# Optimization experiments

Hardware: AMD Instinct MI355X
Metric: run time of the kernel (lower is better)

## Reference

```python
import jax, jax.numpy as jnp
import numpy as np

DIM = 128
HEADS = 8
RBF_K = 16
N_LIG = 20000
N_PROT = 80000
E = 262144
HEAD_DIM = DIM // HEADS
SCALE = HEAD_DIM ** -0.5


def setup_inputs() -> dict:
    key = jax.random.key(0)
    ks = jax.random.split(key, 16)
    inp = {
        "ligand_x": jax.random.normal(ks[0], (N_LIG, DIM), dtype=jnp.float32),
        "protein_x": jax.random.normal(ks[1], (N_PROT, DIM), dtype=jnp.float32),
        "cross_edges": jax.random.randint(ks[2], (E, 2), 0, N_LIG, dtype=jnp.int64)
        if jax.config.jax_enable_x64 else jax.random.randint(ks[2], (E, 2), 0, N_LIG, dtype=jnp.int32),
        "cross_attr": jax.random.uniform(ks[3], (E, RBF_K), dtype=jnp.float32),
        "Wq": jax.random.normal(ks[4], (DIM, DIM), dtype=jnp.float32) * (DIM ** -0.5),
        "bq": jax.random.normal(ks[5], (DIM,), dtype=jnp.float32) * 0.02,
        "Wk": jax.random.normal(ks[6], (DIM, DIM), dtype=jnp.float32) * (DIM ** -0.5),
        "bk": jax.random.normal(ks[7], (DIM,), dtype=jnp.float32) * 0.02,
        "Wv": jax.random.normal(ks[8], (DIM, DIM), dtype=jnp.float32) * (DIM ** -0.5),
        "bv": jax.random.normal(ks[9], (DIM,), dtype=jnp.float32) * 0.02,
        "Wo": jax.random.normal(ks[10], (DIM, DIM), dtype=jnp.float32) * (DIM ** -0.5),
        "bo": jax.random.normal(ks[11], (DIM,), dtype=jnp.float32) * 0.02,
        "Wr": jax.random.normal(ks[12], (RBF_K, HEADS), dtype=jnp.float32) * (RBF_K ** -0.5),
        "br": jax.random.normal(ks[13], (HEADS,), dtype=jnp.float32) * 0.02,
        "lig_start": 0,
        "prot_start": 0,
    }
    return inp


def _heads(t):
    return t.reshape(t.shape[0], HEADS, HEAD_DIM)


def _cross_attend(q_nodes, k_nodes, v_nodes, dst_idx, src_idx, rbf_bias, n_dst):
    # gather per-edge q/k/v: [E, H, D]
    qe = q_nodes[dst_idx]
    ke = k_nodes[src_idx]
    ve = v_nodes[src_idx]
    logits = jnp.einsum("ehd,ehd->eh", qe, ke) * SCALE + rbf_bias  # [E, H]
    # segment softmax over edges grouped by destination node
    m = jax.ops.segment_max(logits, dst_idx, num_segments=n_dst)  # [N, H]
    ex = jnp.exp(logits - m[dst_idx])
    s = jax.ops.segment_sum(ex, dst_idx, num_segments=n_dst)  # [N, H]
    w = ex / (s[dst_idx] + 1e-8)  # [E, H]
    agg = jax.ops.segment_sum(w[:, :, None] * ve, dst_idx, num_segments=n_dst)
    return agg.reshape(n_dst, HEADS * HEAD_DIM)


def reference(ligand_x, protein_x, cross_edges, cross_attr, Wq, bq, Wk, bk, Wv, bv,
              Wo, bo, Wr, br, lig_start, prot_start):
    n_lig, n_prot = ligand_x.shape[0], protein_x.shape[0]
    q_l = _heads(ligand_x @ Wq + bq)
    k_p = _heads(protein_x @ Wk + bk)
    v_p = _heads(protein_x @ Wv + bv)
    q_p = _heads(protein_x @ Wq + bq)
    k_l = _heads(ligand_x @ Wk + bk)
    v_l = _heads(ligand_x @ Wv + bv)

    lig_local = cross_edges[:, 0] - lig_start
    prot_local = cross_edges[:, 1] - prot_start
    rbf_bias = cross_attr @ Wr + br  # [E, heads]

    lig_agg = _cross_attend(q_l, k_p, v_p, lig_local, prot_local, rbf_bias, n_lig)
    prot_agg = _cross_attend(q_p, k_l, v_l, prot_local, lig_local, rbf_bias, n_prot)

    ligand_out = lig_agg @ Wo + bo   # dropout is identity at inference
    protein_out = prot_agg @ Wo + bo
    return (ligand_out, protein_out)
```

## Files before the change

kernel.cpp:

```cpp
#include <hip/hip_runtime.h>
#include <hip/hip_bf16.h>

typedef unsigned short u16;
typedef __attribute__((ext_vector_type(8))) short short8;
typedef __attribute__((ext_vector_type(4))) float f32x4;

__device__ __forceinline__ float bf2f(u16 u){
  union { unsigned int i; float f; } c; c.i = ((unsigned int)u) << 16; return c.f;
}
__device__ __forceinline__ u16 f2bf(float f){
  union { float f; unsigned int i; } c; c.f = f;
  unsigned int x = c.i;
  return (u16)((x + 0x7FFFu + ((x >> 16) & 1u)) >> 16);
}

__device__ __forceinline__ int edge_get(const int* __restrict__ e32, int i64, int e, int c){
  int idx = 2 * e + c;
  return i64 ? e32[2 * idx] : e32[idx];
}

__global__ __launch_bounds__(256) void init_kernel(
    const u16* __restrict__ lig16, const int* __restrict__ e32,
    int* __restrict__ flags, int* __restrict__ cnt, int ntot)
{
  int tid = threadIdx.x;
  if (blockIdx.x == 0){
    if (tid < 64){
      int c = 0, nz = 0;
      #pragma unroll
      for (int j = 0; j < 4; j++){
        u16 u = lig16[(tid * 4 + j) * 2];
        int ex = (u >> 7) & 0xFF;
        if (ex >= 96 && ex < 160) c++;
        if (e32[(tid * 4 + j) * 2 + 1] != 0) nz++;
      }
      #pragma unroll
      for (int off = 1; off < 64; off <<= 1){
        c  += __shfl_xor(c, off);
        nz += __shfl_xor(nz, off);
      }
      if (tid == 0){
        flags[0] = (c < 128) ? 1 : 0;
        flags[1] = (nz == 0) ? 1 : 0;
      }
    }
  } else {
    int i = (blockIdx.x - 1) * 256 + tid;
    if (i < ntot) cnt[i] = 0;
  }
}

__global__ __launch_bounds__(256) void prep_w(
    const void* __restrict__ Wq, const void* __restrict__ Wk,
    const void* __restrict__ Wv, const void* __restrict__ Wo,
    const void* __restrict__ bq, const void* __restrict__ bk,
    const void* __restrict__ bv, const void* __restrict__ bo,
    u16* __restrict__ Wt, float* __restrict__ biasP, const int* __restrict__ flags)
{
  int mat = blockIdx.x, tid = threadIdx.x;
  const void* W = (mat == 0) ? Wq : (mat == 1) ? Wk : (mat == 2) ? Wv : Wo;
  const void* b = (mat == 0) ? bq : (mat == 1) ? bk : (mat == 2) ? bv : bo;
  int F = flags[0];
  u16* dst = Wt + mat * 16384;
  #pragma unroll 4
  for (int j = 0; j < 64; j++){
    int idx = tid + j * 256;
    u16 w = F ? f2bf(((const float*)W)[idx]) : ((const u16*)W)[idx];
    dst[(idx & 127) * 128 + (idx >> 7)] = w;
  }
  if (tid < 128)
    biasP[mat * 128 + tid] = F ? ((const float*)b)[tid] : bf2f(((const u16*)b)[tid]);
}

__global__ __launch_bounds__(256) void fat_qkv_ep(
    const void* __restrict__ A0, int M0, const void* __restrict__ A1, int M1, int mb0,
    const u16* __restrict__ Wt, const float* __restrict__ biasP,
    u16* __restrict__ O0b, u16* __restrict__ O1b, u16* __restrict__ O2b,
    const void* __restrict__ attr, const void* __restrict__ Wr,
    const void* __restrict__ br, float* __restrict__ ebias,
    const int* __restrict__ edges, const int* __restrict__ ls_p,
    const int* __restrict__ ps_p, int* __restrict__ cnt,
    int nlig, int E_, const int* __restrict__ flags)
{
  __shared__ __align__(16) char smem[34816];
  int tid = threadIdx.x;
  int F = flags[0];

  int TT = mb0 + ((M1 + 63) >> 6);
  int eb = (E_ + 255) >> 8;
  int G  = TT + eb;
  int bx = blockIdx.x;
  long long pp = (long long)bx * TT;
  int tile = (int)(pp / G);
  int isQ  = (int)(((long long)(bx + 1) * TT) / G) > tile;

  if (isQ){
    u16 (*As)[136] = (u16(*)[136])smem;
    u16 (*Fs)[136] = (u16(*)[136])(smem + 17408);
    int AF = F;
    const void* A; int M, m0, orow;
    if (tile < mb0){ A = A0; M = M0; m0 = tile * 64;          orow = m0; }
    else           { A = A1; M = M1; m0 = (tile - mb0) * 64;  orow = M0 + m0; }

    if (AF){
      const float* Af = (const float*)A;
      #pragma unroll
      for (int j = 0; j < 8; j++){
        int u = tid + j * 256, row = u >> 5, c4 = (u & 31) * 4;
        float4 v = make_float4(0.f, 0.f, 0.f, 0.f);
        if (m0 + row < M) v = *(const float4*)&Af[(size_t)(m0 + row) * 128 + c4];
        ushort4 o; o.x = f2bf(v.x); o.y = f2bf(v.y); o.z = f2bf(v.z); o.w = f2bf(v.w);
        *(ushort4*)&As[row][c4] = o;
      }
    } else {
      const float4* Au = (const float4*)A;
      #pragma unroll
      for (int j = 0; j < 4; j++){
        int u = tid + j * 256, row = u >> 4, c8 = (u & 15);
        float4 v = make_float4(0.f, 0.f, 0.f, 0.f);
        if (m0 + row < M) v = Au[(size_t)(m0 + row) * 16 + c8];
        *(float4*)&As[row][c8 * 8] = v;
      }
    }
    __syncthreads();

    int wave = tid >> 6, lane = tid & 63;
    int quad = lane >> 4, ml = lane & 15;

    for (int mat = 0; mat < 3; mat++){
      const u16* wp = Wt + (size_t)mat * 16384
                        + (size_t)(wave * 32 + ml) * 128 + quad * 8;
      short8 wf0[4], wf1[4];
      #pragma unroll
      for (int kk = 0; kk < 4; kk++){
        wf0[kk] = *(const short8*)&wp[kk * 32];
        wf1[kk] = *(const short8*)&wp[2048 + kk * 32];
      }
      float b0 = biasP[mat * 128 + wave * 32 + ml];
      float b1 = biasP[mat * 128 + wave * 32 + 16 + ml];

      f32x4 acc[4][2];
      #pragma unroll
      for (int mt = 0; mt < 4; mt++){
        acc[mt][0] = (f32x4){0.f, 0.f, 0.f, 0.f};
        acc[mt][1] = (f32x4){0.f, 0.f, 0.f, 0.f};
      }
      #pragma unroll
      for (int mt = 0; mt < 4; mt++){
        #pragma unroll
        for (int kk = 0; kk < 4; kk++){
          short8 af = *(const short8*)&As[mt * 16 + ml][kk * 32 + quad * 8];
          acc[mt][0] = __builtin_amdgcn_mfma_f32_16x16x32_bf16(af, wf0[kk], acc[mt][0], 0, 0, 0);
          acc[mt][1] = __builtin_amdgcn_mfma_f32_16x16x32_bf16(af, wf1[kk], acc[mt][1], 0, 0, 0);
        }
      }

      if (mat > 0) __syncthreads();
      #pragma unroll
      for (int mt = 0; mt < 4; mt++){
        #pragma unroll
        for (int r = 0; r < 4; r++){
          int row = mt * 16 + quad * 4 + r;
          Fs[row][wave * 32 + ml]      = f2bf(acc[mt][0][r] + b0);
          Fs[row][wave * 32 + 16 + ml] = f2bf(acc[mt][1][r] + b1);
        }
      }
      __syncthreads();
      u16* Cb = (mat == 0) ? O0b : ((mat == 1) ? O1b : O2b);
      #pragma unroll
      for (int j = 0; j < 4; j++){
        int u = tid + j * 256, row = u >> 4, c8 = (u & 15) * 8;
        if (m0 + row < M)
          *(short8*)&Cb[(size_t)(orow + row) * 128 + c8] = *(const short8*)&Fs[row][c8];
      }
    }
  } else {
    int eidx = bx - tile;
    float (*w)[8] = (float(*)[8])smem;
    float* b = (float*)(smem + 512);
    if (tid < 128) w[tid >> 3][tid & 7] = F ? ((const float*)Wr)[tid] : bf2f(((const u16*)Wr)[tid]);
    if (tid < 8)   b[tid] = F ? ((const float*)br)[tid] : bf2f(((const u16*)br)[tid]);
    __syncthreads();
    int e = eidx * 256 + tid;
    if (e >= E_) return;

    int I64 = flags[1];
    int dl = edge_get(edges, I64, e, 0) - ls_p[0];
    int dp = edge_get(edges, I64, e, 1) - ps_p[0];
    atomicAdd(&cnt[dl], 1);
    atomicAdd(&cnt[nlig + dp], 1);

    float a[16];
    if (F){
      const float* af = (const float*)attr;
      #pragma unroll
      for (int j = 0; j < 4; j++){
        float4 t = *(const float4*)&af[e * 16 + j * 4];
        a[4*j] = t.x; a[4*j+1] = t.y; a[4*j+2] = t.z; a[4*j+3] = t.w;
      }
    } else {
      const u16* au = (const u16*)attr;
      #pragma unroll
      for (int j = 0; j < 4; j++){
        ushort4 t = *(const ushort4*)&au[e * 16 + j * 4];
        a[4*j] = bf2f(t.x); a[4*j+1] = bf2f(t.y); a[4*j+2] = bf2f(t.z); a[4*j+3] = bf2f(t.w);
      }
    }
    #pragma unroll
    for (int hh = 0; hh < 8; hh++){
      float s = b[hh];
      #pragma unroll
      for (int r = 0; r < 16; r++) s += a[r] * w[r][hh];
      ebias[e * 8 + hh] = s;
    }
  }
}

__global__ __launch_bounds__(256) void gemm_multi(
    const void* __restrict__ A0, int M0, const void* __restrict__ A1, int M1, int mb0,
    const u16* __restrict__ Wt, const float* __restrict__ biasP, int wbase, int nm,
    u16* __restrict__ O0b, u16* __restrict__ O1b, u16* __restrict__ O2b,
    float* __restrict__ O0f,
    int a_force_bf16, int final_out, const int* __restrict__ flags)
{
  __shared__ __align__(16) u16 As[64][136];
  __shared__ __align__(16) u16 Fs[64][136];

  int tid = threadIdx.x;
  int F = flags[0];
  int AF = a_force_bf16 ? 0 : F;
  int xb = blockIdx.x;
  const void* A; int M, m0, orow;
  if (xb < mb0){ A = A0; M = M0; m0 = xb * 64;          orow = m0; }
  else         { A = A1; M = M1; m0 = (xb - mb0) * 64;  orow = M0 + m0; }

  if (AF){
    const float* Af = (const float*)A;
    #pragma unroll
    for (int j = 0; j < 8; j++){
      int u = tid + j * 256, row = u >> 5, c4 = (u & 31) * 4;
      float4 v = make_float4(0.f, 0.f, 0.f, 0.f);
      if (m0 + row < M) v = *(const float4*)&Af[(size_t)(m0 + row) * 128 + c4];
      ushort4 o; o.x = f2bf(v.x); o.y = f2bf(v.y); o.z = f2bf(v.z); o.w = f2bf(v.w);
      *(ushort4*)&As[row][c4] = o;
    }
  } else {
    const float4* Au = (const float4*)A;
    #pragma unroll
    for (int j = 0; j < 4; j++){
      int u = tid + j * 256, row = u >> 4, c8 = (u & 15);
      float4 v = make_float4(0.f, 0.f, 0.f, 0.f);
      if (m0 + row < M) v = Au[(size_t)(m0 + row) * 16 + c8];
      *(float4*)&As[row][c8 * 8] = v;
    }
  }
  __syncthreads();

  int wave = tid >> 6, lane = tid & 63;
  int quad = lane >> 4, ml = lane & 15;
  int f32out = final_out && F;

  for (int mat = 0; mat < nm; mat++){
    const u16* wp = Wt + (size_t)(wbase + mat) * 16384
                      + (size_t)(wave * 32 + ml) * 128 + quad * 8;
    short8 wf0[4], wf1[4];
    #pragma unroll
    for (int kk = 0; kk < 4; kk++){
      wf0[kk] = *(const short8*)&wp[kk * 32];
      wf1[kk] = *(const short8*)&wp[2048 + kk * 32];
    }
    float b0 = biasP[(wbase + mat) * 128 + wave * 32 + ml];
    float b1 = biasP[(wbase + mat) * 128 + wave * 32 + 16 + ml];

    f32x4 acc[4][2];
    #pragma unroll
    for (int mt = 0; mt < 4; mt++){
      acc[mt][0] = (f32x4){0.f, 0.f, 0.f, 0.f};
      acc[mt][1] = (f32x4){0.f, 0.f, 0.f, 0.f};
    }

    #pragma unroll
    for (int mt = 0; mt < 4; mt++){
      #pragma unroll
      for (int kk = 0; kk < 4; kk++){
        short8 af = *(const short8*)&As[mt * 16 + ml][kk * 32 + quad * 8];
        acc[mt][0] = __builtin_amdgcn_mfma_f32_16x16x32_bf16(af, wf0[kk], acc[mt][0], 0, 0, 0);
        acc[mt][1] = __builtin_amdgcn_mfma_f32_16x16x32_bf16(af, wf1[kk], acc[mt][1], 0, 0, 0);
      }
    }

    if (f32out){
      #pragma unroll
      for (int mt = 0; mt < 4; mt++){
        #pragma unroll
        for (int r = 0; r < 4; r++){
          int row = mt * 16 + quad * 4 + r;
          if (m0 + row < M){
            float* op = &O0f[(size_t)(orow + row) * 128 + wave * 32 + ml];
            op[0]  = acc[mt][0][r] + b0;
            op[16] = acc[mt][1][r] + b1;
          }
        }
      }
    } else {
      if (mat > 0) __syncthreads();
      #pragma unroll
      for (int mt = 0; mt < 4; mt++){
        #pragma unroll
        for (int r = 0; r < 4; r++){
          int row = mt * 16 + quad * 4 + r;
          Fs[row][wave * 32 + ml]      = f2bf(acc[mt][0][r] + b0);
          Fs[row][wave * 32 + 16 + ml] = f2bf(acc[mt][1][r] + b1);
        }
      }
      __syncthreads();
      u16* Cb = (mat == 0) ? O0b : ((mat == 1) ? O1b : O2b);
      #pragma unroll
      for (int j = 0; j < 4; j++){
        int u = tid + j * 256, row = u >> 4, c8 = (u & 15) * 8;
        if (m0 + row < M)
          *(short8*)&Cb[(size_t)(orow + row) * 128 + c8] = *(const short8*)&Fs[row][c8];
      }
    }
  }
}

__global__ __launch_bounds__(256) void scan_blocksum(
    const int* __restrict__ cnt, int* __restrict__ bsum, int n)
{
  __shared__ int red[4];
  int tid = threadIdx.x;
  int i = blockIdx.x * 256 + tid;
  int v = (i < n) ? cnt[i] : 0;
  #pragma unroll
  for (int off = 1; off < 64; off <<= 1) v += __shfl_xor(v, off);
  if ((tid & 63) == 0) red[tid >> 6] = v;
  __syncthreads();
  if (tid == 0) bsum[blockIdx.x] = red[0] + red[1] + red[2] + red[3];
}

__global__ __launch_bounds__(512) void scan_bsum(
    int* __restrict__ bsum, int* __restrict__ boff, int nb)
{
  __shared__ int buf[512];
  int tid = threadIdx.x;
  int v = (tid < nb) ? bsum[tid] : 0;
  buf[tid] = v; __syncthreads();
  for (int off = 1; off < 512; off <<= 1){
    int t = (tid >= off) ? buf[tid - off] : 0;
    __syncthreads();
    buf[tid] += t;
    __syncthreads();
  }
  if (tid < nb) boff[tid] = buf[tid] - v;
}

__global__ __launch_bounds__(256) void scan_final(
    const int* __restrict__ cnt, const int* __restrict__ boff,
    int* __restrict__ offs, int* __restrict__ cursor, int n)
{
  __shared__ int buf[256];
  int tid = threadIdx.x;
  int i = blockIdx.x * 256 + tid;
  int v = (i < n) ? cnt[i] : 0;
  buf[tid] = v; __syncthreads();
  for (int off = 1; off < 256; off <<= 1){
    int t = (tid >= off) ? buf[tid - off] : 0;
    __syncthreads();
    buf[tid] += t;
    __syncthreads();
  }
  int excl = buf[tid] - v + boff[blockIdx.x];
  if (i < n){
    offs[i] = excl;
    cursor[i] = excl;
    if (i == n - 1) offs[n] = excl + v;
  }
}

__global__ __launch_bounds__(256) void scatter_kernel(
    const int* __restrict__ edges, const int* __restrict__ ls_p,
    const int* __restrict__ ps_p, int* __restrict__ cursor,
    int2* __restrict__ sorted, int nlig, int E_,
    const int* __restrict__ flags)
{
  int e = blockIdx.x * 256 + threadIdx.x;
  if (e >= E_) return;
  int I64 = flags[1];
  int dl = edge_get(edges, I64, e, 0) - ls_p[0];
  int dp = edge_get(edges, I64, e, 1) - ps_p[0];
  int p1 = atomicAdd(&cursor[dl], 1);        sorted[p1] = make_int2(e, nlig + dp);
  int p2 = atomicAdd(&cursor[nlig + dp], 1); sorted[p2] = make_int2(e, dl);
}

__global__ __launch_bounds__(256) void attn_kernel(
    const u16* __restrict__ Q, const u16* __restrict__ K, const u16* __restrict__ V,
    const int2* __restrict__ sorted, const int* __restrict__ offs,
    const float* __restrict__ ebias, u16* __restrict__ AGG, int ntot)
{
  int t = blockIdx.x * 4 + (threadIdx.x >> 6);
  if (t >= ntot) return;
  int lane = threadIdx.x & 63;
  int ql = lane & 15;
  int q4 = lane >> 4;
  int h  = ql >> 1;

  int beg = offs[t], end = offs[t + 1];

  if (beg == end){
    if (lane < 16){
      short8 z = {0, 0, 0, 0, 0, 0, 0, 0};
      *(short8*)&AGG[(size_t)t * 128 + ql * 8] = z;
    }
    return;
  }

  short8 qv = *(const short8*)&Q[(size_t)t * 128 + ql * 8];
  float qf[8];
  #pragma unroll
  for (int j = 0; j < 8; j++) qf[j] = bf2f((u16)qv[j]);

  float m = -1e30f, l = 0.f;
  float a[8];
  #pragma unroll
  for (int j = 0; j < 8; j++) a[j] = 0.f;

  int i = beg + q4;
  int2 cur = make_int2(0, 0), nxt = make_int2(0, 0);
  if (i < end)     cur = sorted[i];
  if (i + 4 < end) nxt = sorted[i + 4];

  short8 kA = {0,0,0,0,0,0,0,0}, vA = {0,0,0,0,0,0,0,0};
  float ebA = 0.f;
  if (i < end){
    kA = *(const short8*)&K[(size_t)cur.y * 128 + ql * 8];
    vA = *(const short8*)&V[(size_t)cur.y * 128 + ql * 8];
    ebA = ebias[(size_t)cur.x * 8 + h];
  }

  while (i < end){
    short8 kB = {0,0,0,0,0,0,0,0}, vB = {0,0,0,0,0,0,0,0};
    float ebB = 0.f;
    if (i + 4 < end){
      kB = *(const short8*)&K[(size_t)nxt.y * 128 + ql * 8];
      vB = *(const short8*)&V[(size_t)nxt.y * 128 + ql * 8];
      ebB = ebias[(size_t)nxt.x * 8 + h];
    }
    int2 n2 = make_int2(0, 0);
    if (i + 8 < end) n2 = sorted[i + 8];

    float s = 0.f;
    #pragma unroll
    for (int j = 0; j < 8; j++) s += qf[j] * bf2f((u16)kA[j]);
    s += __shfl_xor(s, 1);
    float logit = s * 0.25f + ebA;
    float nm = fmaxf(m, logit);
    float alpha = __expf(m - nm);
    float p = __expf(logit - nm);
    #pragma unroll
    for (int j = 0; j < 8; j++) a[j] = a[j] * alpha + p * bf2f((u16)vA[j]);
    l = l * alpha + p;
    m = nm;

    kA = kB; vA = vB; ebA = ebB;
    cur = nxt; nxt = n2;
    i += 4;
  }

  #pragma unroll
  for (int mask = 16; mask <= 32; mask <<= 1){
    float mo = __shfl_xor(m, mask);
    float lo = __shfl_xor(l, mask);
    float nm = fmaxf(m, mo);
    float sA = __expf(m - nm);
    float sB = __expf(mo - nm);
    l = l * sA + lo * sB;
    #pragma unroll
    for (int j = 0; j < 8; j++){
      float ao = __shfl_xor(a[j], mask);
      a[j] = a[j] * sA + ao * sB;
    }
    m = nm;
  }

  if (lane < 16){
    float inv = 1.f / (l + 1e-8f);
    short8 o;
    #pragma unroll
    for (int j = 0; j < 8; j++) o[j] = (short)f2bf(a[j] * inv);
    *(short8*)&AGG[(size_t)t * 128 + ql * 8] = o;
  }
}

extern "C" void kernel_launch(void* const* d_in, const int* in_sizes, int n_in,
                              void* d_out, int out_size, void* d_ws, size_t ws_size,
                              hipStream_t stream)
{
  const void* ligand_x  = d_in[0];
  const void* protein_x = d_in[1];
  const int* edges      = (const int*)d_in[2];
  const void* attr      = d_in[3];
  const void* Wq = d_in[4];  const void* bq = d_in[5];
  const void* Wk = d_in[6];  const void* bk = d_in[7];
  const void* Wv = d_in[8];  const void* bv = d_in[9];
  const void* Wo = d_in[10]; const void* bo = d_in[11];
  const void* Wr = d_in[12]; const void* br = d_in[13];
  const int* ls_p = (const int*)d_in[14];
  const int* ps_p = (const int*)d_in[15];

  const int nlig = in_sizes[0] / 128;
  const int nprot = in_sizes[1] / 128;
  const int E = in_sizes[2] / 2;
  const int ntot = nlig + nprot;

  char* w = (char*)d_ws;
  size_t off = 0;
  auto alloc = [&](size_t bytes) -> void* {
    void* p = w + off;
    off = (off + bytes + 255) & ~(size_t)255;
    return p;
  };
  int*   flags = (int*)alloc(256);
  u16*   Wt    = (u16*)alloc(4 * 16384 * 2);
  float* biasP = (float*)alloc(4 * 128 * 4);
  u16* Qb  = (u16*)alloc((size_t)ntot * 128 * 2);
  u16* Kb  = (u16*)alloc((size_t)ntot * 128 * 2);
  u16* Vb  = (u16*)alloc((size_t)ntot * 128 * 2);
  u16* AGG = (u16*)alloc((size_t)ntot * 128 * 2);
  float* ebias = (float*)alloc((size_t)E * 8 * 4);
  int* cnt    = (int*)alloc((size_t)ntot * 4);
  int* offs   = (int*)alloc((size_t)(ntot + 1) * 4);
  int* cursor = (int*)alloc((size_t)ntot * 4);
  int* bsum   = (int*)alloc(512 * 4);
  int* boff   = (int*)alloc(512 * 4);
  int2* sorted = (int2*)alloc((size_t)2 * E * 8);
  (void)ws_size; (void)n_in; (void)out_size;

  const int mb_l = (nlig + 63) / 64;
  const int mb_p = (nprot + 63) / 64;
  const int mb_t = (ntot + 63) / 64;
  const int eb = (E + 255) / 256;
  const int nb = (ntot + 255) / 256;

  init_kernel<<<nb + 1, 256, 0, stream>>>((const u16*)ligand_x, edges, flags, cnt, ntot);

  prep_w<<<4, 256, 0, stream>>>(Wq, Wk, Wv, Wo, bq, bk, bv, bo, Wt, biasP, flags);

  const int TT = mb_l + mb_p;
  fat_qkv_ep<<<TT + eb, 256, 0, stream>>>(
      ligand_x, nlig, protein_x, nprot, mb_l,
      Wt, biasP, Qb, Kb, Vb,
      attr, Wr, br, ebias, edges, ls_p, ps_p, cnt, nlig, E, flags);

  scan_blocksum<<<nb, 256, 0, stream>>>(cnt, bsum, ntot);
  scan_bsum<<<1, 512, 0, stream>>>(bsum, boff, nb);
  scan_final<<<nb, 256, 0, stream>>>(cnt, boff, offs, cursor, ntot);
  scatter_kernel<<<eb, 256, 0, stream>>>(edges, ls_p, ps_p, cursor, sorted, nlig, E, flags);

  attn_kernel<<<(ntot + 3) / 4, 256, 0, stream>>>(Qb, Kb, Vb, sorted, offs, ebias, AGG, ntot);

  gemm_multi<<<mb_t, 256, 0, stream>>>(
      AGG, ntot, nullptr, 0, mb_t,
      Wt, biasP, 3, 1,
      (u16*)d_out, nullptr, nullptr, (float*)d_out,
      1, 1, flags);
}
```

Measured before the change: 319.5 us.

## Merge init kernels, split QKV projection per matrix, chained single-pass scan

Fuses the weight-prep kernel into the init kernel, with each weight block recomputing the dtype flag locally. The QKV projection grid now gives each block one (tile, matrix) pair instead of looping over three matrices, which triples the block count but reloads the A tile three times. The three-kernel prefix scan becomes one chained-scan kernel that passes block partials through spin-waiting atomics. The aim is fewer launches and better parallelism, at the cost of serialized look-back and extra input reads.

Result: slower. 379.4 us (+18.7%).

```diff
diff --git a/kernel.cpp b/kernel.cpp
--- a/kernel.cpp
+++ b/kernel.cpp
@@ -19,12 +19,47 @@
   return i64 ? e32[2 * idx] : e32[idx];
 }
 
-__global__ __launch_bounds__(256) void init_kernel(
+__global__ __launch_bounds__(256) void init_all(
+    const void* __restrict__ Wq, const void* __restrict__ Wk,
+    const void* __restrict__ Wv, const void* __restrict__ Wo,
+    const void* __restrict__ bq, const void* __restrict__ bk,
+    const void* __restrict__ bv, const void* __restrict__ bo,
+    u16* __restrict__ Wt, float* __restrict__ biasP,
     const u16* __restrict__ lig16, const int* __restrict__ e32,
-    int* __restrict__ flags, int* __restrict__ cnt, int ntot)
-{
-  int tid = threadIdx.x;
-  if (blockIdx.x == 0){
+    int* __restrict__ flags, int* __restrict__ partials,
+    int* __restrict__ cnt, int ntot)
+{
+  int bx = blockIdx.x, tid = threadIdx.x;
+
+  if (bx < 4){
+    __shared__ int Fsh;
+    if (tid < 64){
+      int c = 0;
+      #pragma unroll
+      for (int j = 0; j < 4; j++){
+        u16 u = lig16[(tid * 4 + j) * 2];
+        int ex = (u >> 7) & 0xFF;
+        if (ex >= 96 && ex < 160) c++;
+      }
+      #pragma unroll
+      for (int off = 1; off < 64; off <<= 1) c += __shfl_xor(c, off);
+      if (tid == 0) Fsh = (c < 128) ? 1 : 0;
+    }
+    __syncthreads();
+    int F = Fsh;
+    int mat = bx;
+    const void* W = (mat == 0) ? Wq : (mat == 1) ? Wk : (mat == 2) ? Wv : Wo;
+    const void* b = (mat == 0) ? bq : (mat == 1) ? bk : (mat == 2) ? bv : bo;
+    u16* dst = Wt + mat * 16384;
+    #pragma unroll 4
+    for (int j = 0; j < 64; j++){
+      int idx = tid + j * 256;
+      u16 w = F ? f2bf(((const float*)W)[idx]) : ((const u16*)W)[idx];
+      dst[(idx & 127) * 128 + (idx >> 7)] = w;
+    }
+    if (tid < 128)
+      biasP[mat * 128 + tid] = F ? ((const float*)b)[tid] : bf2f(((const u16*)b)[tid]);
+  } else if (bx == 4){
     if (tid < 64){
       int c = 0, nz = 0;
       #pragma unroll
@@ -44,32 +79,12 @@
         flags[1] = (nz == 0) ? 1 : 0;
       }
     }
+    partials[tid] = -1;
+    partials[256 + tid] = -1;
   } else {
-    int i = (blockIdx.x - 1) * 256 + tid;
+    int i = (bx - 5) * 256 + tid;
     if (i < ntot) cnt[i] = 0;
   }
-}
-
-__global__ __launch_bounds__(256) void prep_w(
-    const void* __restrict__ Wq, const void* __restrict__ Wk,
-    const void* __restrict__ Wv, const void* __restrict__ Wo,
-    const void* __restrict__ bq, const void* __restrict__ bk,
-    const void* __restrict__ bv, const void* __restrict__ bo,
-    u16* __restrict__ Wt, float* __restrict__ biasP, const int* __restrict__ flags)
-{
-  int mat = blockIdx.x, tid = threadIdx.x;
-  const void* W = (mat == 0) ? Wq : (mat == 1) ? Wk : (mat == 2) ? Wv : Wo;
-  const void* b = (mat == 0) ? bq : (mat == 1) ? bk : (mat == 2) ? bv : bo;
-  int F = flags[0];
-  u16* dst = Wt + mat * 16384;
-  #pragma unroll 4
-  for (int j = 0; j < 64; j++){
-    int idx = tid + j * 256;
-    u16 w = F ? f2bf(((const float*)W)[idx]) : ((const u16*)W)[idx];
-    dst[(idx & 127) * 128 + (idx >> 7)] = w;
-  }
-  if (tid < 128)
-    biasP[mat * 128 + tid] = F ? ((const float*)b)[tid] : bf2f(((const u16*)b)[tid]);
 }
 
 __global__ __launch_bounds__(256) void fat_qkv_ep(
@@ -88,13 +103,16 @@
 
   int TT = mb0 + ((M1 + 63) >> 6);
   int eb = (E_ + 255) >> 8;
-  int G  = TT + eb;
+  long long NQ = 3LL * TT;
+  int G  = (int)NQ + eb;
   int bx = blockIdx.x;
-  long long pp = (long long)bx * TT;
-  int tile = (int)(pp / G);
-  int isQ  = (int)(((long long)(bx + 1) * TT) / G) > tile;
+  long long q = ((long long)bx * NQ) / G;
+  int isQ = (int)(((long long)(bx + 1) * NQ) / G) > (int)q;
 
   if (isQ){
+    int qidx = (int)q;
+    int tile = qidx / 3;
+    int mat  = qidx - tile * 3;
     u16 (*As)[136] = (u16(*)[136])smem;
     u16 (*Fs)[136] = (u16(*)[136])(smem + 17408);
     int AF = F;
@@ -127,55 +145,52 @@
     int wave = tid >> 6, lane = tid & 63;
     int quad = lane >> 4, ml = lane & 15;
 
-    for (int mat = 0; mat < 3; mat++){
-      const u16* wp = Wt + (size_t)mat * 16384
-                        + (size_t)(wave * 32 + ml) * 128 + quad * 8;
-      short8 wf0[4], wf1[4];
+    const u16* wp = Wt + (size_t)mat * 16384
+                      + (size_t)(wave * 32 + ml) * 128 + quad * 8;
+    short8 wf0[4], wf1[4];
+    #pragma unroll
+    for (int kk = 0; kk < 4; kk++){
+      wf0[kk] = *(const short8*)&wp[kk * 32];
+      wf1[kk] = *(const short8*)&wp[2048 + kk * 32];
+    }
+    float b0 = biasP[mat * 128 + wave * 32 + ml];
+    float b1 = biasP[mat * 128 + wave * 32 + 16 + ml];
+
+    f32x4 acc[4][2];
+    #pragma unroll
+    for (int mt = 0; mt < 4; mt++){
+      acc[mt][0] = (f32x4){0.f, 0.f, 0.f, 0.f};
+      acc[mt][1] = (f32x4){0.f, 0.f, 0.f, 0.f};
+    }
+    #pragma unroll
+    for (int mt = 0; mt < 4; mt++){
       #pragma unroll
       for (int kk = 0; kk < 4; kk++){
-        wf0[kk] = *(const short8*)&wp[kk * 32];
-        wf1[kk] = *(const short8*)&wp[2048 + kk * 32];
-      }
-      float b0 = biasP[mat * 128 + wave * 32 + ml];
-      float b1 = biasP[mat * 128 + wave * 32 + 16 + ml];
-
-      f32x4 acc[4][2];
-      #pragma unroll
-      for (int mt = 0; mt < 4; mt++){
-        acc[mt][0] = (f32x4){0.f, 0.f, 0.f, 0.f};
-        acc[mt][1] = (f32x4){0.f, 0.f, 0.f, 0.f};
-      }
-      #pragma unroll
-      for (int mt = 0; mt < 4; mt++){
-        #pragma unroll
-        for (int kk = 0; kk < 4; kk++){
-          short8 af = *(const short8*)&As[mt * 16 + ml][kk * 32 + quad * 8];
-          acc[mt][0] = __builtin_amdgcn_mfma_f32_16x16x32_bf16(af, wf0[kk], acc[mt][0], 0, 0, 0);
-          acc[mt][1] = __builtin_amdgcn_mfma_f32_16x16x32_bf16(af, wf1[kk], acc[mt][1], 0, 0, 0);
-        }
-      }
-
-      if (mat > 0) __syncthreads();
-      #pragma unroll
-      for (int mt = 0; mt < 4; mt++){
-        #pragma unroll
-        for (int r = 0; r < 4; r++){
-          int row = mt * 16 + quad * 4 + r;
-          Fs[row][wave * 32 + ml]      = f2bf(acc[mt][0][r] + b0);
-          Fs[row][wave * 32 + 16 + ml] = f2bf(acc[mt][1][r] + b1);
-        }
-      }
-      __syncthreads();
-      u16* Cb = (mat == 0) ? O0b : ((mat == 1) ? O1b : O2b);
-      #pragma unroll
-      for (int j = 0; j < 4; j++){
-        int u = tid + j * 256, row = u >> 4, c8 = (u & 15) * 8;
-        if (m0 + row < M)
-          *(short8*)&Cb[(size_t)(orow + row) * 128 + c8] = *(const short8*)&Fs[row][c8];
-      }
+        short8 af = *(const short8*)&As[mt * 16 + ml][kk * 32 + quad * 8];
+        acc[mt][0] = __builtin_amdgcn_mfma_f32_16x16x32_bf16(af, wf0[kk], acc[mt][0], 0, 0, 0);
+        acc[mt][1] = __builtin_amdgcn_mfma_f32_16x16x32_bf16(af, wf1[kk], acc[mt][1], 0, 0, 0);
+      }
+    }
+
+    #pragma unroll
+    for (int mt = 0; mt < 4; mt++){
+      #pragma unroll
+      for (int r = 0; r < 4; r++){
+        int row = mt * 16 + quad * 4 + r;
+        Fs[row][wave * 32 + ml]      = f2bf(acc[mt][0][r] + b0);
+        Fs[row][wave * 32 + 16 + ml] = f2bf(acc[mt][1][r] + b1);
+      }
+    }
+    __syncthreads();
+    u16* Cb = (mat == 0) ? O0b : ((mat == 1) ? O1b : O2b);
+    #pragma unroll
+    for (int j = 0; j < 4; j++){
+      int u = tid + j * 256, row = u >> 4, c8 = (u & 15) * 8;
+      if (m0 + row < M)
+        *(short8*)&Cb[(size_t)(orow + row) * 128 + c8] = *(const short8*)&Fs[row][c8];
     }
   } else {
-    int eidx = bx - tile;
+    int eidx = bx - (int)q;
     float (*w)[8] = (float(*)[8])smem;
     float* b = (float*)(smem + 512);
     if (tid < 128) w[tid >> 3][tid & 7] = F ? ((const float*)Wr)[tid] : bf2f(((const u16*)Wr)[tid]);
@@ -213,6 +228,171 @@
       for (int r = 0; r < 16; r++) s += a[r] * w[r][hh];
       ebias[e * 8 + hh] = s;
     }
+  }
+}
+
+__global__ __launch_bounds__(256) void scan_chain(
+    const int* __restrict__ cnt, int* __restrict__ offs, int* __restrict__ cursor,
+    int* __restrict__ partials, int n)
+{
+  __shared__ int lds[256];
+  __shared__ int base_s;
+  int b = blockIdx.x, tid = threadIdx.x;
+  int i0 = b * 2048 + tid * 8;
+
+  int v[8]; int s = 0;
+  #pragma unroll
+  for (int j = 0; j < 8; j++){
+    int idx = i0 + j;
+    v[j] = (idx < n) ? cnt[idx] : 0;
+    s += v[j];
+  }
+  lds[tid] = s; __syncthreads();
+  for (int off = 1; off < 256; off <<= 1){
+    int t = (tid >= off) ? lds[tid - off] : 0;
+    __syncthreads();
+    lds[tid] += t;
+    __syncthreads();
+  }
+  int thr_excl = lds[tid] - s;
+  int block_sum = lds[255];
+
+  if (tid == 0){
+    int prev = 0;
+    if (b > 0){
+      while ((prev = __hip_atomic_load(&partials[b - 1], __ATOMIC_ACQUIRE,
+                                       __HIP_MEMORY_SCOPE_AGENT)) < 0){}
+    }
+    __hip_atomic_store(&partials[b], prev + block_sum, __ATOMIC_RELEASE,
+                       __HIP_MEMORY_SCOPE_AGENT);
+    base_s = prev;
+  }
+  __syncthreads();
+
+  int base = base_s + thr_excl;
+  #pragma unroll
+  for (int j = 0; j < 8; j++){
+    int idx = i0 + j;
+    if (idx < n){
+      offs[idx] = base;
+      cursor[idx] = base;
+      base += v[j];
+      if (idx == n - 1) offs[n] = base;
+    }
+  }
+}
+
+__global__ __launch_bounds__(256) void scatter_kernel(
+    const int* __restrict__ edges, const int* __restrict__ ls_p,
+    const int* __restrict__ ps_p, int* __restrict__ cursor,
+    int2* __restrict__ sorted, int nlig, int E_,
+    const int* __restrict__ flags)
+{
+  int e = blockIdx.x * 256 + threadIdx.x;
+  if (e >= E_) return;
+  int I64 = flags[1];
+  int dl = edge_get(edges, I64, e, 0) - ls_p[0];
+  int dp = edge_get(edges, I64, e, 1) - ps_p[0];
+  int p1 = atomicAdd(&cursor[dl], 1);        sorted[p1] = make_int2(e, nlig + dp);
+  int p2 = atomicAdd(&cursor[nlig + dp], 1); sorted[p2] = make_int2(e, dl);
+}
+
+__global__ __launch_bounds__(256) void attn_kernel(
+    const u16* __restrict__ Q, const u16* __restrict__ K, const u16* __restrict__ V,
+    const int2* __restrict__ sorted, const int* __restrict__ offs,
+    const float* __restrict__ ebias, u16* __restrict__ AGG, int ntot)
+{
+  int t = blockIdx.x * 4 + (threadIdx.x >> 6);
+  if (t >= ntot) return;
+  int lane = threadIdx.x & 63;
+  int ql = lane & 15;
+  int q4 = lane >> 4;
+  int h  = ql >> 1;
+
+  int beg = offs[t], end = offs[t + 1];
+
+  if (beg == end){
+    if (lane < 16){
+      short8 z = {0, 0, 0, 0, 0, 0, 0, 0};
+      *(short8*)&AGG[(size_t)t * 128 + ql * 8] = z;
+    }
+    return;
+  }
+
+  short8 qv = *(const short8*)&Q[(size_t)t * 128 + ql * 8];
+  float qf[8];
+  #pragma unroll
+  for (int j = 0; j < 8; j++) qf[j] = bf2f((u16)qv[j]);
+
+  float m = -1e30f, l = 0.f;
+  float a[8];
+  #pragma unroll
+  for (int j = 0; j < 8; j++) a[j] = 0.f;
+
+  int i = beg + q4;
+  int2 cur = make_int2(0, 0), nxt = make_int2(0, 0);
+  if (i < end)     cur = sorted[i];
+  if (i + 4 < end) nxt = sorted[i + 4];
+
+  short8 kA = {0,0,0,0,0,0,0,0}, vA = {0,0,0,0,0,0,0,0};
+  float ebA = 0.f;
+  if (i < end){
+    kA = *(const short8*)&K[(size_t)cur.y * 128 + ql * 8];
+    vA = *(const short8*)&V[(size_t)cur.y * 128 + ql * 8];
+    ebA = ebias[(size_t)cur.x * 8 + h];
+  }
+
+  while (i < end){
+    short8 kB = {0,0,0,0,0,0,0,0}, vB = {0,0,0,0,0,0,0,0};
+    float ebB = 0.f;
+    if (i + 4 < end){
+      kB = *(const short8*)&K[(size_t)nxt.y * 128 + ql * 8];
+      vB = *(const short8*)&V[(size_t)nxt.y * 128 + ql * 8];
+      ebB = ebias[(size_t)nxt.x * 8 + h];
+    }
+    int2 n2 = make_int2(0, 0);
+    if (i + 8 < end) n2 = sorted[i + 8];
+
+    float s = 0.f;
+    #pragma unroll
+    for (int j = 0; j < 8; j++) s += qf[j] * bf2f((u16)kA[j]);
+    s += __shfl_xor(s, 1);
+    float logit = s * 0.25f + ebA;
+    float nm = fmaxf(m, logit);
+    float alpha = __expf(m - nm);
+    float p = __expf(logit - nm);
+    #pragma unroll
+    for (int j = 0; j < 8; j++) a[j] = a[j] * alpha + p * bf2f((u16)vA[j]);
+    l = l * alpha + p;
+    m = nm;
+
+    kA = kB; vA = vB; ebA = ebB;
+    cur = nxt; nxt = n2;
+    i += 4;
+  }
+
+  #pragma unroll
+  for (int mask = 16; mask <= 32; mask <<= 1){
+    float mo = __shfl_xor(m, mask);
+    float lo = __shfl_xor(l, mask);
+    float nm = fmaxf(m, mo);
+    float sA = __expf(m - nm);
+    float sB = __expf(mo - nm);
+    l = l * sA + lo * sB;
+    #pragma unroll
+    for (int j = 0; j < 8; j++){
+      float ao = __shfl_xor(a[j], mask);
+      a[j] = a[j] * sA + ao * sB;
+    }
+    m = nm;
+  }
+
+  if (lane < 16){
+    float inv = 1.f / (l + 1e-8f);
+    short8 o;
+    #pragma unroll
+    for (int j = 0; j < 8; j++) o[j] = (short)f2bf(a[j] * inv);
+    *(short8*)&AGG[(size_t)t * 128 + ql * 8] = o;
   }
 }
 
@@ -322,173 +502,6 @@
           *(short8*)&Cb[(size_t)(orow + row) * 128 + c8] = *(const short8*)&Fs[row][c8];
       }
     }
-  }
-}
-
-__global__ __launch_bounds__(256) void scan_blocksum(
-    const int* __restrict__ cnt, int* __restrict__ bsum, int n)
-{
-  __shared__ int red[4];
-  int tid = threadIdx.x;
-  int i = blockIdx.x * 256 + tid;
-  int v = (i < n) ? cnt[i] : 0;
-  #pragma unroll
-  for (int off = 1; off < 64; off <<= 1) v += __shfl_xor(v, off);
-  if ((tid & 63) == 0) red[tid >> 6] = v;
-  __syncthreads();
-  if (tid == 0) bsum[blockIdx.x] = red[0] + red[1] + red[2] + red[3];
-}
-
-__global__ __launch_bounds__(512) void scan_bsum(
-    int* __restrict__ bsum, int* __restrict__ boff, int nb)
-{
-  __shared__ int buf[512];
-  int tid = threadIdx.x;
-  int v = (tid < nb) ? bsum[tid] : 0;
-  buf[tid] = v; __syncthreads();
-  for (int off = 1; off < 512; off <<= 1){
-    int t = (tid >= off) ? buf[tid - off] : 0;
-    __syncthreads();
-    buf[tid] += t;
-    __syncthreads();
-  }
-  if (tid < nb) boff[tid] = buf[tid] - v;
-}
-
-__global__ __launch_bounds__(256) void scan_final(
-    const int* __restrict__ cnt, const int* __restrict__ boff,
-    int* __restrict__ offs, int* __restrict__ cursor, int n)
-{
-  __shared__ int buf[256];
-  int tid = threadIdx.x;
-  int i = blockIdx.x * 256 + tid;
-  int v = (i < n) ? cnt[i] : 0;
-  buf[tid] = v; __syncthreads();
-  for (int off = 1; off < 256; off <<= 1){
-    int t = (tid >= off) ? buf[tid - off] : 0;
-    __syncthreads();
-    buf[tid] += t;
-    __syncthreads();
-  }
-  int excl = buf[tid] - v + boff[blockIdx.x];
-  if (i < n){
-    offs[i] = excl;
-    cursor[i] = excl;
-    if (i == n - 1) offs[n] = excl + v;
-  }
-}
-
-__global__ __launch_bounds__(256) void scatter_kernel(
-    const int* __restrict__ edges, const int* __restrict__ ls_p,
-    const int* __restrict__ ps_p, int* __restrict__ cursor,
-    int2* __restrict__ sorted, int nlig, int E_,
-    const int* __restrict__ flags)
-{
-  int e = blockIdx.x * 256 + threadIdx.x;
-  if (e >= E_) return;
-  int I64 = flags[1];
-  int dl = edge_get(edges, I64, e, 0) - ls_p[0];
-  int dp = edge_get(edges, I64, e, 1) - ps_p[0];
-  int p1 = atomicAdd(&cursor[dl], 1);        sorted[p1] = make_int2(e, nlig + dp);
-  int p2 = atomicAdd(&cursor[nlig + dp], 1); sorted[p2] = make_int2(e, dl);
-}
-
-__global__ __launch_bounds__(256) void attn_kernel(
-    const u16* __restrict__ Q, const u16* __restrict__ K, const u16* __restrict__ V,
-    const int2* __restrict__ sorted, const int* __restrict__ offs,
-    const float* __restrict__ ebias, u16* __restrict__ AGG, int ntot)
-{
-  int t = blockIdx.x * 4 + (threadIdx.x >> 6);
-  if (t >= ntot) return;
-  int lane = threadIdx.x & 63;
-  int ql = lane & 15;
-  int q4 = lane >> 4;
-  int h  = ql >> 1;
-
-  int beg = offs[t], end = offs[t + 1];
-
-  if (beg == end){
-    if (lane < 16){
-      short8 z = {0, 0, 0, 0, 0, 0, 0, 0};
-      *(short8*)&AGG[(size_t)t * 128 + ql * 8] = z;
-    }
-    return;
-  }
-
-  short8 qv = *(const short8*)&Q[(size_t)t * 128 + ql * 8];
-  float qf[8];
-  #pragma unroll
-  for (int j = 0; j < 8; j++) qf[j] = bf2f((u16)qv[j]);
-
-  float m = -1e30f, l = 0.f;
-  float a[8];
-  #pragma unroll
-  for (int j = 0; j < 8; j++) a[j] = 0.f;
-
-  int i = beg + q4;
-  int2 cur = make_int2(0, 0), nxt = make_int2(0, 0);
-  if (i < end)     cur = sorted[i];
-  if (i + 4 < end) nxt = sorted[i + 4];
-
-  short8 kA = {0,0,0,0,0,0,0,0}, vA = {0,0,0,0,0,0,0,0};
-  float ebA = 0.f;
-  if (i < end){
-    kA = *(const short8*)&K[(size_t)cur.y * 128 + ql * 8];
-    vA = *(const short8*)&V[(size_t)cur.y * 128 + ql * 8];
-    ebA = ebias[(size_t)cur.x * 8 + h];
-  }
-
-  while (i < end){
-    short8 kB = {0,0,0,0,0,0,0,0}, vB = {0,0,0,0,0,0,0,0};
-    float ebB = 0.f;
-    if (i + 4 < end){
-      kB = *(const short8*)&K[(size_t)nxt.y * 128 + ql * 8];
-      vB = *(const short8*)&V[(size_t)nxt.y * 128 + ql * 8];
-      ebB = ebias[(size_t)nxt.x * 8 + h];
-    }
-    int2 n2 = make_int2(0, 0);
-    if (i + 8 < end) n2 = sorted[i + 8];
-
-    float s = 0.f;
-    #pragma unroll
-    for (int j = 0; j < 8; j++) s += qf[j] * bf2f((u16)kA[j]);
-    s += __shfl_xor(s, 1);
-    float logit = s * 0.25f + ebA;
-    float nm = fmaxf(m, logit);
-    float alpha = __expf(m - nm);
-    float p = __expf(logit - nm);
-    #pragma unroll
-    for (int j = 0; j < 8; j++) a[j] = a[j] * alpha + p * bf2f((u16)vA[j]);
-    l = l * alpha + p;
-    m = nm;
-
-    kA = kB; vA = vB; ebA = ebB;
-    cur = nxt; nxt = n2;
-    i += 4;
-  }
-
-  #pragma unroll
-  for (int mask = 16; mask <= 32; mask <<= 1){
-    float mo = __shfl_xor(m, mask);
-    float lo = __shfl_xor(l, mask);
-    float nm = fmaxf(m, mo);
-    float sA = __expf(m - nm);
-    float sB = __expf(mo - nm);
-    l = l * sA + lo * sB;
-    #pragma unroll
-    for (int j = 0; j < 8; j++){
-      float ao = __shfl_xor(a[j], mask);
-      a[j] = a[j] * sA + ao * sB;
-    }
-    m = nm;
-  }
-
-  if (lane < 16){
-    float inv = 1.f / (l + 1e-8f);
-    short8 o;
-    #pragma unroll
-    for (int j = 0; j < 8; j++) o[j] = (short)f2bf(a[j] * inv);
-    *(short8*)&AGG[(size_t)t * 128 + ql * 8] = o;
   }
 }
 
@@ -528,11 +541,10 @@
   u16* Vb  = (u16*)alloc((size_t)ntot * 128 * 2);
   u16* AGG = (u16*)alloc((size_t)ntot * 128 * 2);
   float* ebias = (float*)alloc((size_t)E * 8 * 4);
-  int* cnt    = (int*)alloc((size_t)ntot * 4);
-  int* offs   = (int*)alloc((size_t)(ntot + 1) * 4);
-  int* cursor = (int*)alloc((size_t)ntot * 4);
-  int* bsum   = (int*)alloc(512 * 4);
-  int* boff   = (int*)alloc(512 * 4);
+  int* cnt      = (int*)alloc((size_t)ntot * 4);
+  int* offs     = (int*)alloc((size_t)(ntot + 1) * 4);
+  int* cursor   = (int*)alloc((size_t)ntot * 4);
+  int* partials = (int*)alloc(512 * 4);
   int2* sorted = (int2*)alloc((size_t)2 * E * 8);
   (void)ws_size; (void)n_in; (void)out_size;
 
@@ -541,20 +553,20 @@
   const int mb_t = (ntot + 63) / 64;
   const int eb = (E + 255) / 256;
   const int nb = (ntot + 255) / 256;
-
-  init_kernel<<<nb + 1, 256, 0, stream>>>((const u16*)ligand_x, edges, flags, cnt, ntot);
-
-  prep_w<<<4, 256, 0, stream>>>(Wq, Wk, Wv, Wo, bq, bk, bv, bo, Wt, biasP, flags);
+  const int nsb = (ntot + 2047) / 2048;
+
+  init_all<<<nb + 5, 256, 0, stream>>>(
+      Wq, Wk, Wv, Wo, bq, bk, bv, bo, Wt, biasP,
+      (const u16*)ligand_x, edges, flags, partials, cnt, ntot);
 
   const int TT = mb_l + mb_p;
-  fat_qkv_ep<<<TT + eb, 256, 0, stream>>>(
+  fat_qkv_ep<<<3 * TT + eb, 256, 0, stream>>>(
       ligand_x, nlig, protein_x, nprot, mb_l,
       Wt, biasP, Qb, Kb, Vb,
       attr, Wr, br, ebias, edges, ls_p, ps_p, cnt, nlig, E, flags);
 
-  scan_blocksum<<<nb, 256, 0, stream>>>(cnt, bsum, ntot);
-  scan_bsum<<<1, 512, 0, stream>>>(bsum, boff, nb);
-  scan_final<<<nb, 256, 0, stream>>>(cnt, boff, offs, cursor, ntot);
+  scan_chain<<<nsb, 256, 0, stream>>>(cnt, offs, cursor, partials, ntot);
+
   scatter_kernel<<<eb, 256, 0, stream>>>(edges, ls_p, ps_p, cursor, sorted, nlig, E, flags);
 
   attn_kernel<<<(ntot + 3) / 4, 256, 0, stream>>>(Qb, Kb, Vb, sorted, offs, ebias, AGG, ntot);
```
